# Performance work log

Hardware: AMD Instinct MI355X
Metric: run time of the kernel (lower is better)

Reference implementation:

```python
import jax, jax.numpy as jnp
import numpy as np

NUM_ELECTIONS = 4096  # number of segments (elections)
N_VOTERS = 1048576
NUM_CANDIDATES = 32
EMB = 128


def setup_inputs() -> dict:
    key = jax.random.key(0)
    ks = jax.random.split(key, 9)
    s = lambda k, sh: jax.random.normal(k, sh, dtype=jnp.float32) * 0.05
    x = jax.random.normal(ks[0], (N_VOTERS, NUM_CANDIDATES), dtype=jnp.float32)
    index = jnp.sort(jax.random.randint(ks[1], (N_VOTERS,), 0, NUM_ELECTIONS)).astype(jnp.int64)
    return {
        "x": x,
        "index": index,
        "lW1": s(ks[2], (NUM_CANDIDATES, EMB)), "lb1": jnp.zeros((EMB,), jnp.float32),
        "lW2": s(ks[3], (EMB, EMB)),            "lb2": jnp.zeros((EMB,), jnp.float32),
        "lW3": s(ks[4], (EMB, EMB)),            "lb3": jnp.zeros((EMB,), jnp.float32),
        "gW1": s(ks[5], (EMB, EMB)),            "gb1": jnp.zeros((EMB,), jnp.float32),
        "gW2": s(ks[6], (EMB, EMB)),            "gb2": jnp.zeros((EMB,), jnp.float32),
        "gW3": s(ks[7], (EMB, NUM_CANDIDATES)), "gb3": jnp.zeros((NUM_CANDIDATES,), jnp.float32),
    }


def reference(x, index, lW1, lb1, lW2, lb2, lW3, lb3, gW1, gb1, gW2, gb2, gW3, gb3):
    # local_nn per voter row: MLP [C, E, E, E], ReLU on hidden layers, plain last
    h = jax.nn.relu(x @ lW1 + lb1)
    h = jax.nn.relu(h @ lW2 + lb2)
    h = h @ lW3 + lb3                      # [N, E]
    # scatter-sum aggregation by election id (DeepSetsAggregation sum reduce)
    agg = jax.ops.segment_sum(h, index, num_segments=NUM_ELECTIONS)  # [S, E]
    # global_nn: MLP [E, E, E, C]
    g = jax.nn.relu(agg @ gW1 + gb1)
    g = jax.nn.relu(g @ gW2 + gb2)
    scores = g @ gW3 + gb3                 # [S, C]
    return jax.nn.log_softmax(scores, axis=-1)
```

## Files before the change

### kernel.cpp

```cpp
#include <hip/hip_runtime.h>
#include <hip/hip_bf16.h>
#include <math.h>

#define N_VOTERS 1048576
#define NUM_CAND 32
#define EMB 128
#define NUM_ELEC 4096

typedef unsigned short u16;
typedef unsigned int u32;
typedef __attribute__((ext_vector_type(8))) short bf16x8;
typedef __attribute__((ext_vector_type(4))) short short4v;
typedef __attribute__((ext_vector_type(4))) float f32x4;

#if defined(__has_builtin)
#if __has_builtin(__builtin_amdgcn_cvt_pk_bf16_f32)
#define HAVE_CVT_PK_BF16 1
#endif
#endif

__device__ __forceinline__ u16 f2bf(float f) {
    union { float f; u32 u; } v; v.f = f;
    u32 r = v.u + 0x7FFFu + ((v.u >> 16) & 1u);
    return (u16)(r >> 16);
}
__device__ __forceinline__ u32 pk2(float f0, float f1) {
#ifdef HAVE_CVT_PK_BF16
    typedef __attribute__((ext_vector_type(2))) __bf16 bf16x2;
    bf16x2 r = __builtin_amdgcn_cvt_pk_bf16_f32(f0, f1);
    union { bf16x2 v; u32 u; } c; c.v = r;
    return c.u;
#else
    u32 u0 = __float_as_uint(f0) + 0x8000u;
    u32 u1 = __float_as_uint(f1) + 0x8000u;
    return __builtin_amdgcn_perm(u1, u0, 0x07060302u);
#endif
}

__global__ void prep_weights(const float* __restrict__ lW1, const float* __restrict__ lW2,
                             const float* __restrict__ lW3,
                             u16* __restrict__ w1t, u16* __restrict__ w2t, u16* __restrict__ w3t) {
    int tid = blockIdx.x * blockDim.x + threadIdx.x;
    if (tid < 4096) {
        int n = tid >> 5, k = tid & 31;
        w1t[tid] = f2bf(lW1[k * EMB + n]);
    }
    {
        int n = tid >> 7, k = tid & 127;
        w2t[tid] = f2bf(lW2[k * EMB + n]);
        w3t[tid] = f2bf(lW3[k * EMB + n]);
    }
}

__global__ __launch_bounds__(256, 3) void local_fused(
    const float* __restrict__ x, const int* __restrict__ idx,
    const float* __restrict__ lb1, const float* __restrict__ lb2,
    const u16* __restrict__ w1t, const u16* __restrict__ w2t, const u16* __restrict__ w3t,
    float* __restrict__ agg, float* __restrict__ cntf)
{
    constexpr int XSTR = 36;
    constexpr int ASTR = 136;
    __shared__ __align__(16) u16 bufX[2][64 * XSTR];
    __shared__ __align__(16) u16 act1[64 * ASTR];
    __shared__ __align__(16) u16 act2[64 * ASTR];

    const int tid = threadIdx.x;
    const int lane = tid & 63;
    const int wv = tid >> 6;
    const int qd = lane >> 4;
    const int l15 = lane & 15;
    const int f0 = wv * 32;
    const int vbase = blockIdx.x * 512;

    bf16x8 w1a[2], w2a[2][4], w3a[2][4];
    f32x4 b1f[2], b2f[2];
    #pragma unroll
    for (int mt = 0; mt < 2; ++mt) {
        int mrow = f0 + mt * 16 + l15;
        w1a[mt] = *(const bf16x8*)(w1t + mrow * 32 + qd * 8);
        #pragma unroll
        for (int kk = 0; kk < 4; ++kk) {
            w2a[mt][kk] = *(const bf16x8*)(w2t + mrow * 128 + kk * 32 + qd * 8);
            w3a[mt][kk] = *(const bf16x8*)(w3t + mrow * 128 + kk * 32 + qd * 8);
        }
        b1f[mt] = *(const f32x4*)(lb1 + f0 + mt * 16 + qd * 4);
        b2f[mt] = *(const f32x4*)(lb2 + f0 + mt * 16 + qd * 4);
    }

    f32x4 accR[2];
    #pragma unroll
    for (int mt = 0; mt < 2; ++mt) accR[mt] = (f32x4){0.f, 0.f, 0.f, 0.f};
    float cntv = 0.f;
    int cur = idx[vbase];

    auto flush = [&]() {
        #pragma unroll
        for (int d = 1; d < 16; d <<= 1)
            #pragma unroll
            for (int mt = 0; mt < 2; ++mt)
                #pragma unroll
                for (int r = 0; r < 4; ++r) accR[mt][r] += __shfl_xor(accR[mt][r], d, 16);
        if (l15 == 0) {
            float* p = agg + (size_t)cur * EMB + f0 + qd * 4;
            #pragma unroll
            for (int mt = 0; mt < 2; ++mt)
                #pragma unroll
                for (int r = 0; r < 4; ++r) atomicAdd(p + mt * 16 + r, accR[mt][r]);
            if (wv == 0 && qd == 0) atomicAdd(cntf + cur, cntv);
        }
        #pragma unroll
        for (int mt = 0; mt < 2; ++mt) accR[mt] = (f32x4){0.f, 0.f, 0.f, 0.f};
        cntv = 0.f;
    };

    auto loadx = [&](int v0, uint2* xp) {
        const float4* xg = (const float4*)(x + (size_t)v0 * NUM_CAND);
        #pragma unroll
        for (int i = 0; i < 2; ++i) {
            float4 v = xg[i * 256 + tid];
            xp[i].x = pk2(v.x, v.y); xp[i].y = pk2(v.z, v.w);
        }
    };
    auto stagex = [&](u16* dst, const uint2* xp) {
        #pragma unroll
        for (int i = 0; i < 2; ++i) {
            int F = i * 256 + tid, row = F >> 3, c4 = (F & 7) * 4;
            *(uint2*)(dst + row * XSTR + c4) = xp[i];
        }
    };

    uint2 xp[2];
    loadx(vbase, xp);
    stagex(bufX[0], xp);
    loadx(vbase + 64, xp);
    __syncthreads();

    #pragma unroll 1
    for (int g = 0; g < 8; ++g) {
        const int vg = vbase + g * 64;

        int sgv[4];
        #pragma unroll
        for (int nt = 0; nt < 4; ++nt) sgv[nt] = idx[vg + nt * 16 + l15];

        const u16* bx = bufX[g & 1];
        #pragma unroll
        for (int nt = 0; nt < 4; ++nt) {
            int vr = nt * 16 + l15;
            union { bf16x8 v; short4v h[2]; } b;
            b.h[0] = *(const short4v*)(bx + vr * XSTR + qd * 8);
            b.h[1] = *(const short4v*)(bx + vr * XSTR + qd * 8 + 4);
            u16* wr = act1 + vr * ASTR + f0 + qd * 4;
            #pragma unroll
            for (int mt = 0; mt < 2; ++mt) {
                f32x4 a = __builtin_amdgcn_mfma_f32_16x16x32_bf16(w1a[mt], b.v, b1f[mt], 0, 0, 0);
                uint2 s;
                s.x = pk2(fmaxf(a[0], 0.f), fmaxf(a[1], 0.f));
                s.y = pk2(fmaxf(a[2], 0.f), fmaxf(a[3], 0.f));
                *(uint2*)(wr + mt * 16) = s;
            }
        }
        __syncthreads();

        if (g < 7) stagex(bufX[(g + 1) & 1], xp);
        if (g < 6) loadx(vg + 128, xp);

        #pragma unroll
        for (int nt = 0; nt < 4; ++nt) {
            const u16* rd = act1 + (nt * 16 + l15) * ASTR + qd * 8;
            bf16x8 B2[4];
            #pragma unroll
            for (int kk = 0; kk < 4; ++kk) B2[kk] = *(const bf16x8*)(rd + kk * 32);
            u16* wr = act2 + (nt * 16 + l15) * ASTR + f0 + qd * 4;
            #pragma unroll
            for (int mt = 0; mt < 2; ++mt) {
                f32x4 a = b2f[mt];
                #pragma unroll
                for (int kk = 0; kk < 4; ++kk)
                    a = __builtin_amdgcn_mfma_f32_16x16x32_bf16(w2a[mt][kk], B2[kk], a, 0, 0, 0);
                uint2 s;
                s.x = pk2(fmaxf(a[0], 0.f), fmaxf(a[1], 0.f));
                s.y = pk2(fmaxf(a[2], 0.f), fmaxf(a[3], 0.f));
                *(uint2*)(wr + mt * 16) = s;
            }
        }
        __syncthreads();

        #pragma unroll 1
        for (int nt = 0; nt < 4; ++nt) {
            int sg = sgv[nt];
            const u16* rd = act2 + (nt * 16 + l15) * ASTR + qd * 8;
            bf16x8 B3[4];
            #pragma unroll
            for (int kk = 0; kk < 4; ++kk) B3[kk] = *(const bf16x8*)(rd + kk * 32);
            int first = __builtin_amdgcn_readfirstlane(sg);
            bool uni = (__ballot(sg == first) == ~0ull);
            if (uni) {
                if (first != cur) {
                    if (cntv > 0.f) flush();
                    cur = first;
                }
                #pragma unroll
                for (int mt = 0; mt < 2; ++mt) {
                    f32x4 a = accR[mt];
                    #pragma unroll
                    for (int kk = 0; kk < 4; ++kk)
                        a = __builtin_amdgcn_mfma_f32_16x16x32_bf16(w3a[mt][kk], B3[kk], a, 0, 0, 0);
                    accR[mt] = a;
                }
                cntv += 16.f;
            } else {
                if (cntv > 0.f) flush();
                f32x4 D[2];
                #pragma unroll
                for (int mt = 0; mt < 2; ++mt) {
                    f32x4 a = {0.f, 0.f, 0.f, 0.f};
                    #pragma unroll
                    for (int kk = 0; kk < 4; ++kk)
                        a = __builtin_amdgcn_mfma_f32_16x16x32_bf16(w3a[mt][kk], B3[kk], a, 0, 0, 0);
                    D[mt] = a;
                }
                float one = 1.f;
                #pragma unroll
                for (int d = 1; d < 16; d <<= 1) {
                    int so = __shfl_up(sg, d, 16);
                    bool ok = (l15 >= d) && (so == sg);
                    #pragma unroll
                    for (int mt = 0; mt < 2; ++mt)
                        #pragma unroll
                        for (int r = 0; r < 4; ++r) {
                            float o = __shfl_up(D[mt][r], d, 16);
                            if (ok) D[mt][r] += o;
                        }
                    float oc = __shfl_up(one, d, 16);
                    if (ok) one += oc;
                }
                int sgn = __shfl_down(sg, 1, 16);
                bool isend = (l15 == 15) || (sgn != sg);
                if (isend) {
                    float* p = agg + (size_t)sg * EMB + f0 + qd * 4;
                    #pragma unroll
                    for (int mt = 0; mt < 2; ++mt)
                        #pragma unroll
                        for (int r = 0; r < 4; ++r) atomicAdd(p + mt * 16 + r, D[mt][r]);
                    if (wv == 0 && qd == 0) atomicAdd(cntf + sg, one);
                }
                cur = __shfl(sg, 15, 16);
            }
        }
    }
    if (cntv > 0.f) flush();
}

__global__ __launch_bounds__(256) void global_mlp(
    const float* __restrict__ agg, const float* __restrict__ cntf, const float* __restrict__ lb3,
    const float* __restrict__ gW1, const float* __restrict__ gb1,
    const float* __restrict__ gW2, const float* __restrict__ gb2,
    const float* __restrict__ gW3, const float* __restrict__ gb3,
    float* __restrict__ out)
{
    __shared__ float actA[8 * 128];
    __shared__ float actB[8 * 128];
    __shared__ float sc[8 * 32];
    const int tid = threadIdx.x;
    const int s0 = blockIdx.x * 8;

    #pragma unroll
    for (int i = 0; i < 4; ++i) {
        int f = i * 256 + tid;
        actA[f] = agg[(size_t)s0 * 128 + f] + cntf[s0 + (f >> 7)] * lb3[f & 127];
    }
    __syncthreads();

    const int j = tid & 127, g = tid >> 7;
    {
        float acc[4];
        #pragma unroll
        for (int si = 0; si < 4; ++si) acc[si] = gb1[j];
        #pragma unroll 8
        for (int k = 0; k < 128; ++k) {
            float w = gW1[k * 128 + j];
            #pragma unroll
            for (int si = 0; si < 4; ++si) acc[si] += actA[(g * 4 + si) * 128 + k] * w;
        }
        #pragma unroll
        for (int si = 0; si < 4; ++si) actB[(g * 4 + si) * 128 + j] = fmaxf(acc[si], 0.f);
    }
    __syncthreads();
    {
        float acc[4];
        #pragma unroll
        for (int si = 0; si < 4; ++si) acc[si] = gb2[j];
        #pragma unroll 8
        for (int k = 0; k < 128; ++k) {
            float w = gW2[k * 128 + j];
            #pragma unroll
            for (int si = 0; si < 4; ++si) acc[si] += actB[(g * 4 + si) * 128 + k] * w;
        }
        #pragma unroll
        for (int si = 0; si < 4; ++si) actA[(g * 4 + si) * 128 + j] = fmaxf(acc[si], 0.f);
    }
    __syncthreads();
    {
        int c = tid & 31, sg = tid >> 5;
        float a3 = gb3[c];
        #pragma unroll 8
        for (int k = 0; k < 128; ++k) a3 += actA[sg * 128 + k] * gW3[k * 32 + c];
        sc[sg * 32 + c] = a3;
    }
    __syncthreads();
    {
        int c = tid & 31, sg = tid >> 5;
        float v = sc[sg * 32 + c];
        float m = v;
        #pragma unroll
        for (int off = 16; off >= 1; off >>= 1) m = fmaxf(m, __shfl_xor(m, off, 32));
        float e = expf(v - m);
        float sum = e;
        #pragma unroll
        for (int off = 16; off >= 1; off >>= 1) sum += __shfl_xor(sum, off, 32);
        out[(size_t)(s0 + sg) * 32 + c] = (v - m) - logf(sum);
    }
}

extern "C" void kernel_launch(void* const* d_in, const int* in_sizes, int n_in,
                              void* d_out, int out_size, void* d_ws, size_t ws_size,
                              hipStream_t stream) {
    const float* x   = (const float*)d_in[0];
    const int*   idx = (const int*)d_in[1];
    const float* lW1 = (const float*)d_in[2];
    const float* lb1 = (const float*)d_in[3];
    const float* lW2 = (const float*)d_in[4];
    const float* lb2 = (const float*)d_in[5];
    const float* lW3 = (const float*)d_in[6];
    const float* lb3 = (const float*)d_in[7];
    const float* gW1 = (const float*)d_in[8];
    const float* gb1 = (const float*)d_in[9];
    const float* gW2 = (const float*)d_in[10];
    const float* gb2 = (const float*)d_in[11];
    const float* gW3 = (const float*)d_in[12];
    const float* gb3 = (const float*)d_in[13];
    float* out = (float*)d_out;

    float* agg  = (float*)d_ws;
    float* cntf = agg + (size_t)NUM_ELEC * EMB;
    u16* w1t = (u16*)(cntf + NUM_ELEC);
    u16* w2t = w1t + 128 * 32;
    u16* w3t = w2t + 128 * 128;

    hipMemsetAsync(d_ws, 0, ((size_t)NUM_ELEC * EMB + NUM_ELEC) * sizeof(float), stream);
    prep_weights<<<64, 256, 0, stream>>>(lW1, lW2, lW3, w1t, w2t, w3t);
    local_fused<<<N_VOTERS / 512, 256, 0, stream>>>(x, idx, lb1, lb2, w1t, w2t, w3t, agg, cntf);
    global_mlp<<<NUM_ELEC / 8, 256, 0, stream>>>(agg, cntf, lb3, gW1, gb1, gW2, gb2, gW3, gb3, out);
}
```

Before: 300.4 us.

## Feed layer-3 MFMA from layer-2 registers via lane shuffles, dropping act2 LDS

Layer-2 output is no longer written to a shared-memory buffer and read back. Each wave's 32-feature K-slice is redistributed with cross-lane shuffles into a B operand, and layer 3 becomes a split-K computation in which each wave accumulates partial sums for all 128 output features (8 accumulators), later combined by atomics. act1 is double-buffered so one __syncthreads per group can be removed. The cost is more accumulator registers, four times as many atomics per flush, and shuffle overhead, which may reduce occupancy.

```diff
diff --git a/kernel.cpp b/kernel.cpp
--- a/kernel.cpp
+++ b/kernel.cpp
@@ -61,8 +61,7 @@
     constexpr int XSTR = 36;
     constexpr int ASTR = 136;
     __shared__ __align__(16) u16 bufX[2][64 * XSTR];
-    __shared__ __align__(16) u16 act1[64 * ASTR];
-    __shared__ __align__(16) u16 act2[64 * ASTR];
+    __shared__ __align__(16) u16 act1[2][64 * ASTR];
 
     const int tid = threadIdx.x;
     const int lane = tid & 63;
@@ -72,24 +71,25 @@
     const int f0 = wv * 32;
     const int vbase = blockIdx.x * 512;
 
-    bf16x8 w1a[2], w2a[2][4], w3a[2][4];
+    bf16x8 w1a[2], w2a[2][4], w3n[8];
     f32x4 b1f[2], b2f[2];
     #pragma unroll
     for (int mt = 0; mt < 2; ++mt) {
         int mrow = f0 + mt * 16 + l15;
         w1a[mt] = *(const bf16x8*)(w1t + mrow * 32 + qd * 8);
         #pragma unroll
-        for (int kk = 0; kk < 4; ++kk) {
+        for (int kk = 0; kk < 4; ++kk)
             w2a[mt][kk] = *(const bf16x8*)(w2t + mrow * 128 + kk * 32 + qd * 8);
-            w3a[mt][kk] = *(const bf16x8*)(w3t + mrow * 128 + kk * 32 + qd * 8);
-        }
         b1f[mt] = *(const f32x4*)(lb1 + f0 + mt * 16 + qd * 4);
         b2f[mt] = *(const f32x4*)(lb2 + f0 + mt * 16 + qd * 4);
     }
-
-    f32x4 accR[2];
     #pragma unroll
-    for (int mt = 0; mt < 2; ++mt) accR[mt] = (f32x4){0.f, 0.f, 0.f, 0.f};
+    for (int mt = 0; mt < 8; ++mt)
+        w3n[mt] = *(const bf16x8*)(w3t + (mt * 16 + l15) * 128 + f0 + qd * 8);
+
+    f32x4 accR[8];
+    #pragma unroll
+    for (int mt = 0; mt < 8; ++mt) accR[mt] = (f32x4){0.f, 0.f, 0.f, 0.f};
     float cntv = 0.f;
     int cur = idx[vbase];
 
@@ -97,19 +97,19 @@
         #pragma unroll
         for (int d = 1; d < 16; d <<= 1)
             #pragma unroll
-            for (int mt = 0; mt < 2; ++mt)
+            for (int mt = 0; mt < 8; ++mt)
                 #pragma unroll
                 for (int r = 0; r < 4; ++r) accR[mt][r] += __shfl_xor(accR[mt][r], d, 16);
         if (l15 == 0) {
-            float* p = agg + (size_t)cur * EMB + f0 + qd * 4;
-            #pragma unroll
-            for (int mt = 0; mt < 2; ++mt)
+            float* p = agg + (size_t)cur * EMB + qd * 4;
+            #pragma unroll
+            for (int mt = 0; mt < 8; ++mt)
                 #pragma unroll
                 for (int r = 0; r < 4; ++r) atomicAdd(p + mt * 16 + r, accR[mt][r]);
             if (wv == 0 && qd == 0) atomicAdd(cntf + cur, cntv);
         }
         #pragma unroll
-        for (int mt = 0; mt < 2; ++mt) accR[mt] = (f32x4){0.f, 0.f, 0.f, 0.f};
+        for (int mt = 0; mt < 8; ++mt) accR[mt] = (f32x4){0.f, 0.f, 0.f, 0.f};
         cntv = 0.f;
     };
 
@@ -144,13 +144,14 @@
         for (int nt = 0; nt < 4; ++nt) sgv[nt] = idx[vg + nt * 16 + l15];
 
         const u16* bx = bufX[g & 1];
+        u16* a1w = act1[g & 1];
         #pragma unroll
         for (int nt = 0; nt < 4; ++nt) {
             int vr = nt * 16 + l15;
             union { bf16x8 v; short4v h[2]; } b;
             b.h[0] = *(const short4v*)(bx + vr * XSTR + qd * 8);
             b.h[1] = *(const short4v*)(bx + vr * XSTR + qd * 8 + 4);
-            u16* wr = act1 + vr * ASTR + f0 + qd * 4;
+            u16* wr = a1w + vr * ASTR + f0 + qd * 4;
             #pragma unroll
             for (int mt = 0; mt < 2; ++mt) {
                 f32x4 a = __builtin_amdgcn_mfma_f32_16x16x32_bf16(w1a[mt], b.v, b1f[mt], 0, 0, 0);
@@ -160,39 +161,42 @@
                 *(uint2*)(wr + mt * 16) = s;
             }
         }
-        __syncthreads();
-
         if (g < 7) stagex(bufX[(g + 1) & 1], xp);
         if (g < 6) loadx(vg + 128, xp);
-
-        #pragma unroll
+        __syncthreads();
+
+        const u16* a1r = act1[g & 1];
+        #pragma unroll 2
         for (int nt = 0; nt < 4; ++nt) {
-            const u16* rd = act1 + (nt * 16 + l15) * ASTR + qd * 8;
+            const u16* rd = a1r + (nt * 16 + l15) * ASTR + qd * 8;
             bf16x8 B2[4];
             #pragma unroll
             for (int kk = 0; kk < 4; ++kk) B2[kk] = *(const bf16x8*)(rd + kk * 32);
-            u16* wr = act2 + (nt * 16 + l15) * ASTR + f0 + qd * 4;
-            #pragma unroll
-            for (int mt = 0; mt < 2; ++mt) {
-                f32x4 a = b2f[mt];
-                #pragma unroll
-                for (int kk = 0; kk < 4; ++kk)
-                    a = __builtin_amdgcn_mfma_f32_16x16x32_bf16(w2a[mt][kk], B2[kk], a, 0, 0, 0);
-                uint2 s;
-                s.x = pk2(fmaxf(a[0], 0.f), fmaxf(a[1], 0.f));
-                s.y = pk2(fmaxf(a[2], 0.f), fmaxf(a[3], 0.f));
-                *(uint2*)(wr + mt * 16) = s;
-            }
-        }
-        __syncthreads();
-
-        #pragma unroll 1
-        for (int nt = 0; nt < 4; ++nt) {
+            f32x4 a0 = b2f[0], a1v = b2f[1];
+            #pragma unroll
+            for (int kk = 0; kk < 4; ++kk)
+                a0 = __builtin_amdgcn_mfma_f32_16x16x32_bf16(w2a[0][kk], B2[kk], a0, 0, 0, 0);
+            #pragma unroll
+            for (int kk = 0; kk < 4; ++kk)
+                a1v = __builtin_amdgcn_mfma_f32_16x16x32_bf16(w2a[1][kk], B2[kk], a1v, 0, 0, 0);
+            u32 p0 = pk2(fmaxf(a0[0], 0.f),  fmaxf(a0[1], 0.f));
+            u32 p1 = pk2(fmaxf(a0[2], 0.f),  fmaxf(a0[3], 0.f));
+            u32 p2 = pk2(fmaxf(a1v[0], 0.f), fmaxf(a1v[1], 0.f));
+            u32 p3 = pk2(fmaxf(a1v[2], 0.f), fmaxf(a1v[3], 0.f));
+            int lA = ((2 * qd) & 3) * 16 + l15;
+            int lB = ((2 * qd + 1) & 3) * 16 + l15;
+            u32 a0s = __shfl(p0, lA, 64), a1s = __shfl(p1, lA, 64);
+            u32 a2s = __shfl(p2, lA, 64), a3s = __shfl(p3, lA, 64);
+            u32 b0s = __shfl(p0, lB, 64), b1s = __shfl(p1, lB, 64);
+            u32 b2s = __shfl(p2, lB, 64), b3s = __shfl(p3, lB, 64);
+            bool lo = (qd < 2);
+            union { bf16x8 v; u32 w[4]; } B3;
+            B3.w[0] = lo ? a0s : a2s;
+            B3.w[1] = lo ? a1s : a3s;
+            B3.w[2] = lo ? b0s : b2s;
+            B3.w[3] = lo ? b1s : b3s;
+
             int sg = sgv[nt];
-            const u16* rd = act2 + (nt * 16 + l15) * ASTR + qd * 8;
-            bf16x8 B3[4];
-            #pragma unroll
-            for (int kk = 0; kk < 4; ++kk) B3[kk] = *(const bf16x8*)(rd + kk * 32);
             int first = __builtin_amdgcn_readfirstlane(sg);
             bool uni = (__ballot(sg == first) == ~0ull);
             if (uni) {
@@ -201,50 +205,50 @@
                     cur = first;
                 }
                 #pragma unroll
-                for (int mt = 0; mt < 2; ++mt) {
-                    f32x4 a = accR[mt];
-                    #pragma unroll
-                    for (int kk = 0; kk < 4; ++kk)
-                        a = __builtin_amdgcn_mfma_f32_16x16x32_bf16(w3a[mt][kk], B3[kk], a, 0, 0, 0);
-                    accR[mt] = a;
-                }
+                for (int mt = 0; mt < 8; ++mt)
+                    accR[mt] = __builtin_amdgcn_mfma_f32_16x16x32_bf16(w3n[mt], B3.v, accR[mt], 0, 0, 0);
                 cntv += 16.f;
             } else {
                 if (cntv > 0.f) flush();
-                f32x4 D[2];
-                #pragma unroll
-                for (int mt = 0; mt < 2; ++mt) {
-                    f32x4 a = {0.f, 0.f, 0.f, 0.f};
-                    #pragma unroll
-                    for (int kk = 0; kk < 4; ++kk)
-                        a = __builtin_amdgcn_mfma_f32_16x16x32_bf16(w3a[mt][kk], B3[kk], a, 0, 0, 0);
-                    D[mt] = a;
-                }
                 float one = 1.f;
                 #pragma unroll
                 for (int d = 1; d < 16; d <<= 1) {
                     int so = __shfl_up(sg, d, 16);
                     bool ok = (l15 >= d) && (so == sg);
-                    #pragma unroll
-                    for (int mt = 0; mt < 2; ++mt)
-                        #pragma unroll
-                        for (int r = 0; r < 4; ++r) {
-                            float o = __shfl_up(D[mt][r], d, 16);
-                            if (ok) D[mt][r] += o;
-                        }
                     float oc = __shfl_up(one, d, 16);
                     if (ok) one += oc;
                 }
                 int sgn = __shfl_down(sg, 1, 16);
                 bool isend = (l15 == 15) || (sgn != sg);
-                if (isend) {
-                    float* p = agg + (size_t)sg * EMB + f0 + qd * 4;
+                #pragma unroll
+                for (int h = 0; h < 2; ++h) {
+                    f32x4 D[4];
                     #pragma unroll
-                    for (int mt = 0; mt < 2; ++mt)
+                    for (int m4 = 0; m4 < 4; ++m4) {
+                        f32x4 z = {0.f, 0.f, 0.f, 0.f};
+                        D[m4] = __builtin_amdgcn_mfma_f32_16x16x32_bf16(w3n[h * 4 + m4], B3.v, z, 0, 0, 0);
+                    }
+                    #pragma unroll
+                    for (int d = 1; d < 16; d <<= 1) {
+                        int so = __shfl_up(sg, d, 16);
+                        bool ok = (l15 >= d) && (so == sg);
                         #pragma unroll
-                        for (int r = 0; r < 4; ++r) atomicAdd(p + mt * 16 + r, D[mt][r]);
-                    if (wv == 0 && qd == 0) atomicAdd(cntf + sg, one);
+                        for (int m4 = 0; m4 < 4; ++m4)
+                            #pragma unroll
+                            for (int r = 0; r < 4; ++r) {
+                                float o = __shfl_up(D[m4][r], d, 16);
+                                if (ok) D[m4][r] += o;
+                            }
+                    }
+                    if (isend) {
+                        float* p = agg + (size_t)sg * EMB + h * 64 + qd * 4;
+                        #pragma unroll
+                        for (int m4 = 0; m4 < 4; ++m4)
+                            #pragma unroll
+                            for (int r = 0; r < 4; ++r) atomicAdd(p + m4 * 16 + r, D[m4][r]);
+                    }
                 }
+                if (isend && wv == 0 && qd == 0) atomicAdd(cntf + sg, one);
                 cur = __shfl(sg, 15, 16);
             }
         }
@@ -252,7 +256,7 @@
     if (cntv > 0.f) flush();
 }
 
-__global__ __launch_bounds__(256) void global_mlp(
+__global__ void __launch_bounds__(256) global_mlp(
     const float* __restrict__ agg, const float* __restrict__ cntf, const float* __restrict__ lb3,
     const float* __restrict__ gW1, const float* __restrict__ gb1,
     const float* __restrict__ gW2, const float* __restrict__ gb2,
```

Result: slower. 617.7 us (+105.6%).

## Split feature dimension across 8 waves with 512-thread blocks in local MLP

Applied to the files above, without the earlier changes.

The local fused kernel now launches 512 threads (8 waves) per block, and each wave owns 16 output features instead of 32. Per-wave weight registers, accumulators and MFMA work halve, and each thread loads one x float4 per step instead of two. The intent is more waves in flight to hide memory and LDS latency. The cost is twice as many flush atomics per segment, since each wave commits its own slice, plus more block-wide barrier participants.

```diff
diff --git a/kernel.cpp b/kernel.cpp
--- a/kernel.cpp
+++ b/kernel.cpp
@@ -52,7 +52,7 @@
     }
 }
 
-__global__ __launch_bounds__(256, 3) void local_fused(
+__global__ __launch_bounds__(512, 6) void local_fused(
     const float* __restrict__ x, const int* __restrict__ idx,
     const float* __restrict__ lb1, const float* __restrict__ lb2,
     const u16* __restrict__ w1t, const u16* __restrict__ w2t, const u16* __restrict__ w3t,
@@ -69,27 +69,24 @@
     const int wv = tid >> 6;
     const int qd = lane >> 4;
     const int l15 = lane & 15;
-    const int f0 = wv * 32;
+    const int f0 = wv * 16;
     const int vbase = blockIdx.x * 512;
 
-    bf16x8 w1a[2], w2a[2][4], w3a[2][4];
-    f32x4 b1f[2], b2f[2];
-    #pragma unroll
-    for (int mt = 0; mt < 2; ++mt) {
-        int mrow = f0 + mt * 16 + l15;
-        w1a[mt] = *(const bf16x8*)(w1t + mrow * 32 + qd * 8);
+    bf16x8 w1a, w2a[4], w3a[4];
+    f32x4 b1f, b2f;
+    {
+        int mrow = f0 + l15;
+        w1a = *(const bf16x8*)(w1t + mrow * 32 + qd * 8);
         #pragma unroll
         for (int kk = 0; kk < 4; ++kk) {
-            w2a[mt][kk] = *(const bf16x8*)(w2t + mrow * 128 + kk * 32 + qd * 8);
-            w3a[mt][kk] = *(const bf16x8*)(w3t + mrow * 128 + kk * 32 + qd * 8);
-        }
-        b1f[mt] = *(const f32x4*)(lb1 + f0 + mt * 16 + qd * 4);
-        b2f[mt] = *(const f32x4*)(lb2 + f0 + mt * 16 + qd * 4);
-    }
-
-    f32x4 accR[2];
-    #pragma unroll
-    for (int mt = 0; mt < 2; ++mt) accR[mt] = (f32x4){0.f, 0.f, 0.f, 0.f};
+            w2a[kk] = *(const bf16x8*)(w2t + mrow * 128 + kk * 32 + qd * 8);
+            w3a[kk] = *(const bf16x8*)(w3t + mrow * 128 + kk * 32 + qd * 8);
+        }
+        b1f = *(const f32x4*)(lb1 + f0 + qd * 4);
+        b2f = *(const f32x4*)(lb2 + f0 + qd * 4);
+    }
+
+    f32x4 accR = (f32x4){0.f, 0.f, 0.f, 0.f};
     float cntv = 0.f;
     int cur = idx[vbase];
 
@@ -97,42 +94,31 @@
         #pragma unroll
         for (int d = 1; d < 16; d <<= 1)
             #pragma unroll
-            for (int mt = 0; mt < 2; ++mt)
-                #pragma unroll
-                for (int r = 0; r < 4; ++r) accR[mt][r] += __shfl_xor(accR[mt][r], d, 16);
+            for (int r = 0; r < 4; ++r) accR[r] += __shfl_xor(accR[r], d, 16);
         if (l15 == 0) {
             float* p = agg + (size_t)cur * EMB + f0 + qd * 4;
             #pragma unroll
-            for (int mt = 0; mt < 2; ++mt)
-                #pragma unroll
-                for (int r = 0; r < 4; ++r) atomicAdd(p + mt * 16 + r, accR[mt][r]);
+            for (int r = 0; r < 4; ++r) atomicAdd(p + r, accR[r]);
             if (wv == 0 && qd == 0) atomicAdd(cntf + cur, cntv);
         }
-        #pragma unroll
-        for (int mt = 0; mt < 2; ++mt) accR[mt] = (f32x4){0.f, 0.f, 0.f, 0.f};
+        accR = (f32x4){0.f, 0.f, 0.f, 0.f};
         cntv = 0.f;
     };
 
-    auto loadx = [&](int v0, uint2* xp) {
-        const float4* xg = (const float4*)(x + (size_t)v0 * NUM_CAND);
-        #pragma unroll
-        for (int i = 0; i < 2; ++i) {
-            float4 v = xg[i * 256 + tid];
-            xp[i].x = pk2(v.x, v.y); xp[i].y = pk2(v.z, v.w);
-        }
+    auto loadx = [&](int v0) -> uint2 {
+        float4 v = ((const float4*)(x + (size_t)v0 * NUM_CAND))[tid];
+        uint2 r; r.x = pk2(v.x, v.y); r.y = pk2(v.z, v.w);
+        return r;
     };
-    auto stagex = [&](u16* dst, const uint2* xp) {
-        #pragma unroll
-        for (int i = 0; i < 2; ++i) {
-            int F = i * 256 + tid, row = F >> 3, c4 = (F & 7) * 4;
-            *(uint2*)(dst + row * XSTR + c4) = xp[i];
-        }
+    auto stagex = [&](u16* dst, uint2 xpv) {
+        int row = tid >> 3, c4 = (tid & 7) * 4;
+        *(uint2*)(dst + row * XSTR + c4) = xpv;
     };
 
-    uint2 xp[2];
-    loadx(vbase, xp);
+    uint2 xp;
+    xp = loadx(vbase);
     stagex(bufX[0], xp);
-    loadx(vbase + 64, xp);
+    xp = loadx(vbase + 64);
     __syncthreads();
 
     #pragma unroll 1
@@ -150,20 +136,16 @@
             union { bf16x8 v; short4v h[2]; } b;
             b.h[0] = *(const short4v*)(bx + vr * XSTR + qd * 8);
             b.h[1] = *(const short4v*)(bx + vr * XSTR + qd * 8 + 4);
-            u16* wr = act1 + vr * ASTR + f0 + qd * 4;
-            #pragma unroll
-            for (int mt = 0; mt < 2; ++mt) {
-                f32x4 a = __builtin_amdgcn_mfma_f32_16x16x32_bf16(w1a[mt], b.v, b1f[mt], 0, 0, 0);
-                uint2 s;
-                s.x = pk2(fmaxf(a[0], 0.f), fmaxf(a[1], 0.f));
-                s.y = pk2(fmaxf(a[2], 0.f), fmaxf(a[3], 0.f));
-                *(uint2*)(wr + mt * 16) = s;
-            }
+            f32x4 a = __builtin_amdgcn_mfma_f32_16x16x32_bf16(w1a, b.v, b1f, 0, 0, 0);
+            uint2 s;
+            s.x = pk2(fmaxf(a[0], 0.f), fmaxf(a[1], 0.f));
+            s.y = pk2(fmaxf(a[2], 0.f), fmaxf(a[3], 0.f));
+            *(uint2*)(act1 + vr * ASTR + f0 + qd * 4) = s;
         }
         __syncthreads();
 
         if (g < 7) stagex(bufX[(g + 1) & 1], xp);
-        if (g < 6) loadx(vg + 128, xp);
+        if (g < 6) xp = loadx(vg + 128);
 
         #pragma unroll
         for (int nt = 0; nt < 4; ++nt) {
@@ -171,18 +153,14 @@
             bf16x8 B2[4];
             #pragma unroll
             for (int kk = 0; kk < 4; ++kk) B2[kk] = *(const bf16x8*)(rd + kk * 32);
-            u16* wr = act2 + (nt * 16 + l15) * ASTR + f0 + qd * 4;
-            #pragma unroll
-            for (int mt = 0; mt < 2; ++mt) {
-                f32x4 a = b2f[mt];
-                #pragma unroll
-                for (int kk = 0; kk < 4; ++kk)
-                    a = __builtin_amdgcn_mfma_f32_16x16x32_bf16(w2a[mt][kk], B2[kk], a, 0, 0, 0);
-                uint2 s;
-                s.x = pk2(fmaxf(a[0], 0.f), fmaxf(a[1], 0.f));
-                s.y = pk2(fmaxf(a[2], 0.f), fmaxf(a[3], 0.f));
-                *(uint2*)(wr + mt * 16) = s;
-            }
+            f32x4 a = b2f;
+            #pragma unroll
+            for (int kk = 0; kk < 4; ++kk)
+                a = __builtin_amdgcn_mfma_f32_16x16x32_bf16(w2a[kk], B2[kk], a, 0, 0, 0);
+            uint2 s;
+            s.x = pk2(fmaxf(a[0], 0.f), fmaxf(a[1], 0.f));
+            s.y = pk2(fmaxf(a[2], 0.f), fmaxf(a[3], 0.f));
+            *(uint2*)(act2 + (nt * 16 + l15) * ASTR + f0 + qd * 4) = s;
         }
         __syncthreads();
 
@@ -200,38 +178,28 @@
                     if (cntv > 0.f) flush();
                     cur = first;
                 }
+                f32x4 a = accR;
                 #pragma unroll
-                for (int mt = 0; mt < 2; ++mt) {
-                    f32x4 a = accR[mt];
-                    #pragma unroll
-                    for (int kk = 0; kk < 4; ++kk)
-                        a = __builtin_amdgcn_mfma_f32_16x16x32_bf16(w3a[mt][kk], B3[kk], a, 0, 0, 0);
-                    accR[mt] = a;
-                }
+                for (int kk = 0; kk < 4; ++kk)
+                    a = __builtin_amdgcn_mfma_f32_16x16x32_bf16(w3a[kk], B3[kk], a, 0, 0, 0);
+                accR = a;
                 cntv += 16.f;
             } else {
                 if (cntv > 0.f) flush();
-                f32x4 D[2];
+                f32x4 D = {0.f, 0.f, 0.f, 0.f};
                 #pragma unroll
-                for (int mt = 0; mt < 2; ++mt) {
-                    f32x4 a = {0.f, 0.f, 0.f, 0.f};
-                    #pragma unroll
-                    for (int kk = 0; kk < 4; ++kk)
-                        a = __builtin_amdgcn_mfma_f32_16x16x32_bf16(w3a[mt][kk], B3[kk], a, 0, 0, 0);
-                    D[mt] = a;
-                }
+                for (int kk = 0; kk < 4; ++kk)
+                    D = __builtin_amdgcn_mfma_f32_16x16x32_bf16(w3a[kk], B3[kk], D, 0, 0, 0);
                 float one = 1.f;
                 #pragma unroll
                 for (int d = 1; d < 16; d <<= 1) {
                     int so = __shfl_up(sg, d, 16);
                     bool ok = (l15 >= d) && (so == sg);
                     #pragma unroll
-                    for (int mt = 0; mt < 2; ++mt)
-                        #pragma unroll
-                        for (int r = 0; r < 4; ++r) {
-                            float o = __shfl_up(D[mt][r], d, 16);
-                            if (ok) D[mt][r] += o;
-                        }
+                    for (int r = 0; r < 4; ++r) {
+                        float o = __shfl_up(D[r], d, 16);
+                        if (ok) D[r] += o;
+                    }
                     float oc = __shfl_up(one, d, 16);
                     if (ok) one += oc;
                 }
@@ -240,9 +208,7 @@
                 if (isend) {
                     float* p = agg + (size_t)sg * EMB + f0 + qd * 4;
                     #pragma unroll
-                    for (int mt = 0; mt < 2; ++mt)
-                        #pragma unroll
-                        for (int r = 0; r < 4; ++r) atomicAdd(p + mt * 16 + r, D[mt][r]);
+                    for (int r = 0; r < 4; ++r) atomicAdd(p + r, D[r]);
                     if (wv == 0 && qd == 0) atomicAdd(cntf + sg, one);
                 }
                 cur = __shfl(sg, 15, 16);
@@ -252,7 +218,7 @@
     if (cntv > 0.f) flush();
 }
 
-__global__ __launch_bounds__(256) void global_mlp(
+__global__ void __launch_bounds__(256) global_mlp(
     const float* __restrict__ agg, const float* __restrict__ cntf, const float* __restrict__ lb3,
     const float* __restrict__ gW1, const float* __restrict__ gb1,
     const float* __restrict__ gW2, const float* __restrict__ gb2,
@@ -350,6 +316,6 @@
 
     hipMemsetAsync(d_ws, 0, ((size_t)NUM_ELEC * EMB + NUM_ELEC) * sizeof(float), stream);
     prep_weights<<<64, 256, 0, stream>>>(lW1, lW2, lW3, w1t, w2t, w3t);
-    local_fused<<<N_VOTERS / 512, 256, 0, stream>>>(x, idx, lb1, lb2, w1t, w2t, w3t, agg, cntf);
+    local_fused<<<N_VOTERS / 512, 512, 0, stream>>>(x, idx, lb1, lb2, w1t, w2t, w3t, agg, cntf);
     global_mlp<<<NUM_ELEC / 8, 256, 0, stream>>>(agg, cntf, lb3, gW1, gb1, gW2, gb2, gW3, gb3, out);
 }
```

Result: slower. 456.2 us (+51.9%).
